# Kernel tuning notes

Hardware: AMD Instinct MI355X
Metric: run time of the kernel (lower is better)

Reference implementation:

```python
import jax, jax.numpy as jnp
import numpy as np

BS, SL, N_AGENTS, OBS_DIM, STATE_DIM, N_EDGES, HID = 32, 512, 32, 96, 1024, 64, 256


def _hgcn(w_line, x, H):
    # x: [B, n, 1]; H: [B, n, E]. Faithful to torch HGCN:
    # A = D^{-1/2} H |W| B^{-1} H^T D^{-1/2}, with D, B built from detached H/|W|,
    # inf entries (from 0^{-1} / 0^{-0.5}) zeroed. Diagonal matmuls are implicit scalings.
    w_abs = jnp.abs(w_line)
    Hd = jax.lax.stop_gradient(H)
    d = jnp.einsum('bne,e->bn', Hd, jax.lax.stop_gradient(w_abs))  # [B, n]
    d_is = jnp.where(d > 0, jax.lax.rsqrt(jnp.where(d > 0, d, 1.0)), 0.0)
    b = jnp.sum(Hd, axis=-2)  # [B, E]
    b_inv = jnp.where(b > 0, 1.0 / jnp.where(b > 0, b, 1.0), 0.0)
    t = d_is[..., None] * x                       # D^{-1/2} x
    s = jnp.einsum('bne,bnk->bek', H, t)          # H^T (...)
    s = s * (w_abs[None, :] * b_inv)[..., None]   # |W| B^{-1} (diagonals commute)
    y = jnp.einsum('bne,bek->bnk', H, s)          # H (...)
    return d_is[..., None] * y                    # D^{-1/2} (...)


def _mlp(x, w1, b1, w2, b2):
    return jax.nn.relu(x @ w1 + b1) @ w2 + b2


def setup_inputs() -> dict:
    key = jax.random.key(0)
    ks = jax.random.split(key, 24)
    f = jax.random.normal
    inp = {
        'agent_qs': f(ks[0], (BS, SL, N_AGENTS), jnp.float32),
        'states': f(ks[1], (BS, SL, STATE_DIM), jnp.float32),
        'indiv_us': f(ks[2], (BS, SL, N_AGENTS, OBS_DIM), jnp.float32),
        'edge_W': f(ks[3], (OBS_DIM, N_EDGES), jnp.float32) * 0.1,
        'edge_b': f(ks[4], (N_EDGES,), jnp.float32) * 0.1,
        'wline1': 1.0 + 0.1 * f(ks[5], (N_EDGES,), jnp.float32),
        'wline2': 1.0 + 0.1 * f(ks[6], (N_EDGES,), jnp.float32),
    }
    names = ['hw1', 'hc1', 'hw', 'hc']
    outs = [N_AGENTS, N_AGENTS, N_AGENTS, 1]
    for i, (nm, od) in enumerate(zip(names, outs)):
        inp[nm + '_w1'] = f(ks[7 + 4 * i], (STATE_DIM, HID), jnp.float32) * 0.05
        inp[nm + '_b1'] = f(ks[8 + 4 * i], (HID,), jnp.float32) * 0.05
        inp[nm + '_w2'] = f(ks[9 + 4 * i], (HID, od), jnp.float32) * 0.05
        inp[nm + '_b2'] = f(ks[10 + 4 * i], (od,), jnp.float32) * 0.05
    return inp


def reference(agent_qs, states, indiv_us, edge_W, edge_b, wline1, wline2,
              hw1_w1, hw1_b1, hw1_w2, hw1_b2, hc1_w1, hc1_b1, hc1_w2, hc1_b2,
              hw_w1, hw_b1, hw_w2, hw_b2, hc_w1, hc_b1, hc_w2, hc_b2):
    bs, sl, n = agent_qs.shape
    q = agent_qs.reshape(-1, n)                               # [B, n]
    u = indiv_us.reshape(-1, n, indiv_us.shape[-1])           # [B, n, obs]
    s = states.reshape(-1, states.shape[-1])                  # [B, state_dim]
    H = jax.nn.relu(u @ edge_W + edge_b)                      # hyper_edge_net -> [B, n, E]
    x = q[..., None]                                          # node_features [B, n, 1]
    qs_tot = _hgcn(wline2, _hgcn(wline1, x, H), H)[..., 0]    # two stacked HGCN encoders
    w1 = jnp.abs(_mlp(s, hw1_w1, hw1_b1, hw1_w2, hw1_b2))
    c1 = _mlp(s, hc1_w1, hc1_b1, hc1_w2, hc1_b2)
    qt = jax.nn.elu(qs_tot * w1 + c1)
    w = jnp.abs(_mlp(s, hw_w1, hw_b1, hw_w2, hw_b2))
    c = _mlp(s, hc_w1, hc_b1, hc_w2, hc_b2)[..., 0]
    q_tot = jnp.sum(qt * w, axis=-1) + c
    return q_tot.reshape(bs, sl, 1)
```

## Files before the change

### kernel.cpp

```cpp
#include <hip/hip_runtime.h>
#include <cstdint>

typedef _Float16 f16;
typedef _Float16 f16x2 __attribute__((ext_vector_type(2)));
typedef _Float16 f16x4 __attribute__((ext_vector_type(4)));
typedef _Float16 f16x8 __attribute__((ext_vector_type(8)));
typedef float f32x4 __attribute__((ext_vector_type(4)));

#define AS1U const __attribute__((address_space(1))) unsigned int
#define AS3U __attribute__((address_space(3))) unsigned int

__device__ __forceinline__ void gload_lds16(const void* g, void* l) {
    __builtin_amdgcn_global_load_lds((AS1U*)g, (AS3U*)l, 16, 0, 0);
}

#define WSYNC() asm volatile("s_waitcnt lgkmcnt(0)" ::: "memory")
#define CFENCE() asm volatile("" ::: "memory")

#define BATCH 16384
#define NAG   32
#define OBS   96
#define SDIM  1024
#define NE    64
#define HIDN  256
#define NH    1024

#define NB_ST 1024
#define NB_PW 256
#define NB_SM 101
#define NB_FRONT (NB_ST + NB_PW + NB_SM)

__global__ __launch_bounds__(256) void k_front(
    const float* __restrict__ states,
    const float* __restrict__ w1a, const float* __restrict__ w1b,
    const float* __restrict__ w1c, const float* __restrict__ w1d,
    const float* __restrict__ b1a, const float* __restrict__ b1b,
    const float* __restrict__ b1c, const float* __restrict__ b1d,
    const float* __restrict__ w2a, const float* __restrict__ w2b,
    const float* __restrict__ w2c, const float* __restrict__ w2d,
    f16* __restrict__ states16, f16* __restrict__ W1t, float* __restrict__ b1cat,
    f16* __restrict__ W2t, f16* __restrict__ hcw2) {
    __shared__ float tile[64 * 65];
    const int tid = threadIdx.x;
    int bid = blockIdx.x;

    if (bid < NB_ST) {
        int i = bid * 256 + tid;
        const int n4 = BATCH * SDIM / 4;
        const int stride = NB_ST * 256;
        for (; i < n4; i += stride) {
            float4 v = ((const float4*)states)[i];
            f16x4 h = { (f16)v.x, (f16)v.y, (f16)v.z, (f16)v.w };
            ((f16x4*)states16)[i] = h;
        }
        return;
    }
    bid -= NB_ST;
    if (bid < NB_PW) {
        int mlp = bid >> 6, rem = bid & 63, kt = rem >> 2, ct = rem & 3;
        const float* src = (mlp == 0) ? w1a : (mlp == 1) ? w1b : (mlp == 2) ? w1c : w1d;
        int k0 = kt * 64, c0 = ct * 64;
        for (int i = tid; i < 4096; i += 256) {
            int kk = i >> 6, cc = i & 63;
            tile[kk * 65 + cc] = src[(size_t)(k0 + kk) * 256 + c0 + cc];
        }
        __syncthreads();
        for (int i = tid; i < 4096; i += 256) {
            int cc = i >> 6, kk = i & 63;
            W1t[(size_t)(mlp * 256 + c0 + cc) * 1024 + k0 + kk] = (f16)tile[kk * 65 + cc];
        }
        return;
    }
    bid -= NB_PW;
    {
        int i = bid * 256 + tid;
        if (i < 24576) {
            int mp = i >> 13, rem = i & 8191, oo = rem >> 8, kk = rem & 255;
            const float* src = (mp == 0) ? w2a : (mp == 1) ? w2b : w2c;
            W2t[i] = (f16)src[kk * 32 + oo];
        } else if (i < 24832) {
            int k = i - 24576;
            hcw2[k] = (f16)w2d[k];
        } else if (i < 25856) {
            int n = i - 24832;
            int mlp = n >> 8, c = n & 255;
            const float* bsrc = (mlp == 0) ? b1a : (mlp == 1) ? b1b : (mlp == 2) ? b1c : b1d;
            b1cat[n] = bsrc[c];
        }
    }
}

__global__ __launch_bounds__(512) void k_gemm(
    const f16* __restrict__ A, const f16* __restrict__ B,
    const float* __restrict__ b1cat, const f16* __restrict__ W2t,
    const f16* __restrict__ hcw2, float* __restrict__ Pp) {
    __shared__ __align__(16) char smem[131072];
    f16* Asb = (f16*)smem;
    f16* Bsb = (f16*)(smem + 65536);
    f16* Ts  = (f16*)smem;

    const int tid = threadIdx.x;
    const int w = tid >> 6, l = tid & 63;
    const int lm = l & 15, lk = l >> 4;
    const int wm = w >> 2, wn = w & 3;
    const int p = blockIdx.x;
    const int xcd = p & 7, s = p >> 3;
    const int mt = xcd * 8 + (s >> 2);
    const int nt = s & 3;
    const int m0 = mt * 256, n0 = nt * 256;
    const int c0 = w * 4;
    const int srow = l >> 3;
    const int gchunk = (l & 7) ^ srow;

    float bj[4];
    #pragma unroll
    for (int j = 0; j < 4; j++) bj[j] = b1cat[n0 + wn * 64 + j * 16 + lm];

    f32x4 acc[8][4];
    #pragma unroll
    for (int i = 0; i < 8; i++)
        #pragma unroll
        for (int j = 0; j < 4; j++) acc[i][j] = (f32x4){0.f, 0.f, 0.f, 0.f};

#define STAGE(KT, BI)                                                                     \
    {                                                                                     \
        f16* Ad = Asb + (BI) * 16384;                                                     \
        f16* Bd = Bsb + (BI) * 16384;                                                     \
        _Pragma("unroll")                                                                 \
        for (int i_ = 0; i_ < 4; i_++) {                                                  \
            int cc = c0 + i_;                                                             \
            gload_lds16(&A[(size_t)(m0 + cc * 8 + srow) * 1024 + (KT) * 64 + gchunk * 8], \
                        &Ad[cc * 512]);                                                   \
            gload_lds16(&B[(size_t)(n0 + cc * 8 + srow) * 1024 + (KT) * 64 + gchunk * 8], \
                        &Bd[cc * 512]);                                                   \
        }                                                                                 \
    }

    STAGE(0, 0);
    STAGE(1, 1);

    for (int kt = 0; kt < 16; kt++) {
        if (kt < 15) { asm volatile("s_waitcnt vmcnt(8)" ::: "memory"); }
        else         { asm volatile("s_waitcnt vmcnt(0)" ::: "memory"); }
        CFENCE(); __builtin_amdgcn_s_barrier(); CFENCE();

        const f16* As_ = Asb + (kt & 1) * 16384;
        const f16* Bs_ = Bsb + (kt & 1) * 16384;
        const int swlo = ((lk ^ (lm & 7)) << 3);
        const int swhi = (((4 + lk) ^ (lm & 7)) << 3);

        f16x8 af[4][2], bf01[2][2], bf23[2][2];

        #pragma unroll
        for (int i = 0; i < 4; i++) {
            af[i][0] = *(const f16x8*)&As_[(wm * 128 + i * 16 + lm) * 64 + swlo];
            af[i][1] = *(const f16x8*)&As_[(wm * 128 + i * 16 + lm) * 64 + swhi];
        }
        #pragma unroll
        for (int j = 0; j < 2; j++) {
            bf01[j][0] = *(const f16x8*)&Bs_[(wn * 64 + j * 16 + lm) * 64 + swlo];
            bf01[j][1] = *(const f16x8*)&Bs_[(wn * 64 + j * 16 + lm) * 64 + swhi];
        }
        __builtin_amdgcn_s_setprio(1);
        #pragma unroll
        for (int ks = 0; ks < 2; ks++)
            #pragma unroll
            for (int i = 0; i < 4; i++)
                #pragma unroll
                for (int j = 0; j < 2; j++)
                    acc[i][j] = __builtin_amdgcn_mfma_f32_16x16x32_f16(af[i][ks], bf01[j][ks], acc[i][j], 0, 0, 0);
        __builtin_amdgcn_s_setprio(0);
        CFENCE(); __builtin_amdgcn_s_barrier(); CFENCE();

        #pragma unroll
        for (int j = 0; j < 2; j++) {
            bf23[j][0] = *(const f16x8*)&Bs_[(wn * 64 + (2 + j) * 16 + lm) * 64 + swlo];
            bf23[j][1] = *(const f16x8*)&Bs_[(wn * 64 + (2 + j) * 16 + lm) * 64 + swhi];
        }
        __builtin_amdgcn_s_setprio(1);
        #pragma unroll
        for (int ks = 0; ks < 2; ks++)
            #pragma unroll
            for (int i = 0; i < 4; i++)
                #pragma unroll
                for (int j = 0; j < 2; j++)
                    acc[i][2 + j] = __builtin_amdgcn_mfma_f32_16x16x32_f16(af[i][ks], bf23[j][ks], acc[i][2 + j], 0, 0, 0);
        __builtin_amdgcn_s_setprio(0);
        CFENCE(); __builtin_amdgcn_s_barrier(); CFENCE();

        #pragma unroll
        for (int i = 0; i < 4; i++) {
            af[i][0] = *(const f16x8*)&As_[(wm * 128 + (4 + i) * 16 + lm) * 64 + swlo];
            af[i][1] = *(const f16x8*)&As_[(wm * 128 + (4 + i) * 16 + lm) * 64 + swhi];
        }
        __builtin_amdgcn_s_setprio(1);
        #pragma unroll
        for (int ks = 0; ks < 2; ks++)
            #pragma unroll
            for (int i = 0; i < 4; i++)
                #pragma unroll
                for (int j = 0; j < 2; j++)
                    acc[4 + i][j] = __builtin_amdgcn_mfma_f32_16x16x32_f16(af[i][ks], bf01[j][ks], acc[4 + i][j], 0, 0, 0);
        __builtin_amdgcn_s_setprio(0);
        CFENCE(); __builtin_amdgcn_s_barrier(); CFENCE();

        if (kt < 14) STAGE(kt + 2, kt & 1);
        __builtin_amdgcn_s_setprio(1);
        #pragma unroll
        for (int ks = 0; ks < 2; ks++)
            #pragma unroll
            for (int i = 0; i < 4; i++)
                #pragma unroll
                for (int j = 0; j < 2; j++)
                    acc[4 + i][2 + j] = __builtin_amdgcn_mfma_f32_16x16x32_f16(af[i][ks], bf23[j][ks], acc[4 + i][2 + j], 0, 0, 0);
        __builtin_amdgcn_s_setprio(0);
    }
#undef STAGE

    __syncthreads();

    const int mlp = nt;
    #pragma unroll
    for (int pass = 0; pass < 2; pass++) {
        if (wm == pass) {
            #pragma unroll
            for (int i = 0; i < 8; i++)
                #pragma unroll
                for (int r = 0; r < 4; r++) {
                    int rl = i * 16 + lk * 4 + r;
                    #pragma unroll
                    for (int j = 0; j < 4; j++) {
                        float v = acc[i][j][r] + bj[j];
                        Ts[rl * 264 + wn * 64 + j * 16 + lm] = (f16)(v > 0.f ? v : 0.f);
                    }
                }
        }
        __syncthreads();
        const int grow = m0 + pass * 128 + w * 16;
        if (mlp < 3) {
            const f16* wb = W2t + mlp * 8192;
            f32x4 acc2[2];
            acc2[0] = (f32x4){0, 0, 0, 0}; acc2[1] = (f32x4){0, 0, 0, 0};
            #pragma unroll
            for (int ks = 0; ks < 8; ks++) {
                f16x8 a  = *(const f16x8*)&Ts[(w * 16 + lm) * 264 + ks * 32 + lk * 8];
                f16x8 b0 = *(const f16x8*)&wb[lm * 256 + ks * 32 + lk * 8];
                f16x8 b1 = *(const f16x8*)&wb[(16 + lm) * 256 + ks * 32 + lk * 8];
                acc2[0] = __builtin_amdgcn_mfma_f32_16x16x32_f16(a, b0, acc2[0], 0, 0, 0);
                acc2[1] = __builtin_amdgcn_mfma_f32_16x16x32_f16(a, b1, acc2[1], 0, 0, 0);
            }
            #pragma unroll
            for (int j2 = 0; j2 < 2; j2++)
                #pragma unroll
                for (int r = 0; r < 4; r++)
                    Pp[(size_t)(grow + lk * 4 + r) * 104 + mlp * 32 + j2 * 16 + lm] = acc2[j2][r];
        } else {
            f32x4 acc2 = (f32x4){0, 0, 0, 0};
            #pragma unroll
            for (int ks = 0; ks < 8; ks++) {
                f16x8 a = *(const f16x8*)&Ts[(w * 16 + lm) * 264 + ks * 32 + lk * 8];
                f16x8 bz = (f16x8){0, 0, 0, 0, 0, 0, 0, 0};
                if (lm == 0) bz = *(const f16x8*)&hcw2[ks * 32 + lk * 8];
                acc2 = __builtin_amdgcn_mfma_f32_16x16x32_f16(a, bz, acc2, 0, 0, 0);
            }
            if (lm == 0)
                #pragma unroll
                for (int r = 0; r < 4; r++)
                    Pp[(size_t)(grow + lk * 4 + r) * 104 + 96] = acc2[r];
        }
        if (pass == 0) __syncthreads();
    }
}

__global__ __launch_bounds__(256) void k_hgcn_ep(
    const float* __restrict__ agent_qs, const float* __restrict__ indiv_us,
    const float* __restrict__ edge_W, const float* __restrict__ edge_b,
    const float* __restrict__ wline1, const float* __restrict__ wline2,
    const float* __restrict__ Pp,
    const float* __restrict__ hw1_b2, const float* __restrict__ hc1_b2,
    const float* __restrict__ hw_b2, const float* __restrict__ hc_b2,
    float* __restrict__ out) {
    __shared__ __align__(16) char arena[34304];
    f16*   eWs   = (f16*)arena;
    float* swa   = (float*)(arena + 13312);
    f16*   HsB   = (f16*)(arena + 13824);
    float* svB   = (float*)(arena + 30720);
    float* sttB  = (float*)(arena + 31744);
    float* sdisB = (float*)(arena + 32256);
    float* sbinvB= (float*)(arena + 33280);

    const int tid = threadIdx.x;
    const int w = tid >> 6, l = tid & 63;
    const int b = blockIdx.x * 4 + w;
    f16*   Hw    = HsB + w * (32 * 66);
    float* sv    = svB + w * 64;
    float* stt   = sttB + w * 32;
    float* sdis  = sdisB + w * 64;
    float* sbinv = sbinvB + w * 64;

    const int nn = l & 31, half = l >> 5;

    float pa0 = 0.f, pc0 = 0.f, pw0 = 0.f;
    float p96a = 0.f, bw1 = 0.f, bc1 = 0.f, bww = 0.f, bhc = 0.f;
    if (half == 0) {
        const float* p0 = Pp + (size_t)b * 104;
        pa0 = p0[nn];
        pc0 = p0[32 + nn];
        pw0 = p0[64 + nn];
        p96a = p0[96];
        bw1 = hw1_b2[nn];  bc1 = hc1_b2[nn];
        bww = hw_b2[nn];   bhc = hc_b2[0];
    }
    float q = agent_qs[(size_t)b * 32 + nn];

    for (int i = tid; i < 6144; i += 256) {
        int k = i >> 6, n = i & 63;
        eWs[n * 104 + k] = (f16)edge_W[i];
    }
    if (tid < 64) swa[tid] = fabsf(wline1[tid]);
    else if (tid < 128) swa[tid] = fabsf(wline2[tid - 64]);
    __syncthreads();

    const int lm = l & 15, lk = l >> 4;
    const float* ub = indiv_us + (size_t)b * (NAG * OBS);

    #pragma unroll
    for (int mt = 0; mt < 2; mt++) {
        f16x8 af[3];
        #pragma unroll
        for (int ks = 0; ks < 3; ks++) {
            const float* up = ub + (mt * 16 + lm) * 96 + ks * 32 + lk * 8;
            float4 v0 = *(const float4*)up;
            float4 v1 = *(const float4*)(up + 4);
            af[ks] = (f16x8){ (f16)v0.x, (f16)v0.y, (f16)v0.z, (f16)v0.w,
                              (f16)v1.x, (f16)v1.y, (f16)v1.z, (f16)v1.w };
        }
        #pragma unroll
        for (int nt = 0; nt < 4; nt++) {
            f32x4 acc = {0.f, 0.f, 0.f, 0.f};
            #pragma unroll
            for (int ks = 0; ks < 3; ks++) {
                f16x8 bb = *(const f16x8*)&eWs[(nt * 16 + lm) * 104 + ks * 32 + lk * 8];
                acc = __builtin_amdgcn_mfma_f32_16x16x32_f16(af[ks], bb, acc, 0, 0, 0);
            }
            int col = nt * 16 + lm;
            float bias = edge_b[col];
            #pragma unroll
            for (int r = 0; r < 4; r++) {
                int row = mt * 16 + lk * 4 + r;
                float hv = acc[r] + bias;
                Hw[row * 66 + col] = (f16)(hv > 0.f ? hv : 0.f);
            }
        }
    }
    WSYNC();

    float bsum = 0.f;
    #pragma unroll
    for (int n = 0; n < 32; n++) bsum += (float)Hw[n * 66 + l];
    sbinv[l] = bsum > 0.f ? 1.f / bsum : 0.f;

    float dd = 0.f;
    #pragma unroll 8
    for (int e2 = 0; e2 < 32; e2++) {
        f16x2 h2 = *(const f16x2*)&Hw[nn * 66 + e2 * 2];
        dd += (float)h2.x * swa[half * 64 + e2 * 2] + (float)h2.y * swa[half * 64 + e2 * 2 + 1];
    }
    float dis = dd > 0.f ? rsqrtf(dd) : 0.f;
    sdis[l] = dis;
    if (half == 0) stt[nn] = dis * q;
    WSYNC();

    float s1 = 0.f;
    #pragma unroll
    for (int n = 0; n < 32; n++) s1 += (float)Hw[n * 66 + l] * stt[n];
    sv[l] = s1 * swa[l] * sbinv[l];
    WSYNC();

    float y1 = 0.f;
    #pragma unroll 8
    for (int e2 = 0; e2 < 32; e2++) {
        f16x2 h2 = *(const f16x2*)&Hw[nn * 66 + e2 * 2];
        y1 += (float)h2.x * sv[e2 * 2] + (float)h2.y * sv[e2 * 2 + 1];
    }
    float x2 = sdis[nn] * y1;
    if (half == 0) stt[nn] = sdis[32 + nn] * x2;
    WSYNC();

    float s2 = 0.f;
    #pragma unroll
    for (int n = 0; n < 32; n++) s2 += (float)Hw[n * 66 + l] * stt[n];
    sv[l] = s2 * swa[64 + l] * sbinv[l];
    WSYNC();

    float y2 = 0.f;
    #pragma unroll 8
    for (int e2 = 0; e2 < 32; e2++) {
        f16x2 h2 = *(const f16x2*)&Hw[nn * 66 + e2 * 2];
        y2 += (float)h2.x * sv[e2 * 2] + (float)h2.y * sv[e2 * 2 + 1];
    }

    float qsv = sdis[32 + nn] * y2;
    float w1v = fabsf(pa0 + bw1);
    float c1v = pc0 + bc1;
    float wwv = fabsf(pw0 + bww);
    float z = qsv * w1v + c1v;
    float qt = z > 0.f ? z : expm1f(z);
    float val = (half == 0) ? qt * wwv : 0.f;
    val += __shfl_xor(val, 1, 32);
    val += __shfl_xor(val, 2, 32);
    val += __shfl_xor(val, 4, 32);
    val += __shfl_xor(val, 8, 32);
    val += __shfl_xor(val, 16, 32);
    if (l == 0) out[b] = val + p96a + bhc;
}

extern "C" void kernel_launch(void* const* d_in, const int* in_sizes, int n_in,
                              void* d_out, int out_size, void* d_ws, size_t ws_size,
                              hipStream_t stream) {
    const float* agent_qs = (const float*)d_in[0];
    const float* states   = (const float*)d_in[1];
    const float* indiv_us = (const float*)d_in[2];
    const float* edge_W   = (const float*)d_in[3];
    const float* edge_b   = (const float*)d_in[4];
    const float* wline1   = (const float*)d_in[5];
    const float* wline2   = (const float*)d_in[6];
    const float* hw1_w1 = (const float*)d_in[7];
    const float* hw1_b1 = (const float*)d_in[8];
    const float* hw1_w2 = (const float*)d_in[9];
    const float* hw1_b2 = (const float*)d_in[10];
    const float* hc1_w1 = (const float*)d_in[11];
    const float* hc1_b1 = (const float*)d_in[12];
    const float* hc1_w2 = (const float*)d_in[13];
    const float* hc1_b2 = (const float*)d_in[14];
    const float* hw_w1  = (const float*)d_in[15];
    const float* hw_b1  = (const float*)d_in[16];
    const float* hw_w2  = (const float*)d_in[17];
    const float* hw_b2  = (const float*)d_in[18];
    const float* hc_w1  = (const float*)d_in[19];
    const float* hc_b1  = (const float*)d_in[20];
    const float* hc_w2  = (const float*)d_in[21];
    const float* hc_b2  = (const float*)d_in[22];

    char* ws = (char*)d_ws;
    size_t o_states16 = 0;
    size_t o_W1t  = o_states16 + (size_t)BATCH * SDIM * 2;
    size_t o_b1   = o_W1t + (size_t)NH * SDIM * 2;
    size_t o_W2t  = o_b1 + 4096;
    size_t o_hcw2 = o_W2t + 49152;
    size_t o_Pp   = o_hcw2 + 512;

    f16*   states16 = (f16*)(ws + o_states16);
    f16*   W1t      = (f16*)(ws + o_W1t);
    float* b1cat    = (float*)(ws + o_b1);
    f16*   W2t      = (f16*)(ws + o_W2t);
    f16*   hcw2     = (f16*)(ws + o_hcw2);
    float* Pp       = (float*)(ws + o_Pp);

    k_front<<<NB_FRONT, 256, 0, stream>>>(
        states,
        hw1_w1, hc1_w1, hw_w1, hc_w1, hw1_b1, hc1_b1, hw_b1, hc_b1,
        hw1_w2, hc1_w2, hw_w2, hc_w2,
        states16, W1t, b1cat, W2t, hcw2);
    k_gemm<<<256, 512, 0, stream>>>(states16, W1t, b1cat, W2t, hcw2, Pp);
    k_hgcn_ep<<<BATCH / 4, 256, 0, stream>>>(
        agent_qs, indiv_us, edge_W, edge_b, wline1, wline2, Pp,
        hw1_b2, hc1_b2, hw_b2, hc_b2, (float*)d_out);
}
```

Baseline: 120.4 us.

## Process four samples per wave in HGCN kernel with register prefetch

Each wave now handles four consecutive batch samples instead of one, with the grid shrunk accordingly. This amortizes the per-block edge_W conversion into LDS. While one sample is being computed, the indiv_us tile, Pp entries and agent_qs values for the next sample are loaded into registers so global latency overlaps compute. The cost is more live registers (48 floats for the prefetch buffer), which may lower occupancy, and fewer blocks to spread across the device.

New measurement: 131.5 us. 9.2% more time.

```diff
diff --git a/kernel.cpp b/kernel.cpp
--- a/kernel.cpp
+++ b/kernel.cpp
@@ -291,7 +291,7 @@
 
     const int tid = threadIdx.x;
     const int w = tid >> 6, l = tid & 63;
-    const int b = blockIdx.x * 4 + w;
+    const int b0 = blockIdx.x * 16 + w * 4;
     f16*   Hw    = HsB + w * (32 * 66);
     float* sv    = svB + w * 64;
     float* stt   = sttB + w * 32;
@@ -299,19 +299,28 @@
     float* sbinv = sbinvB + w * 64;
 
     const int nn = l & 31, half = l >> 5;
-
-    float pa0 = 0.f, pc0 = 0.f, pw0 = 0.f;
-    float p96a = 0.f, bw1 = 0.f, bc1 = 0.f, bww = 0.f, bhc = 0.f;
+    const int lm = l & 15, lk = l >> 4;
+
+    float4 uf[2][3][2];
+    {
+        const float* ub = indiv_us + (size_t)b0 * (NAG * OBS);
+        #pragma unroll
+        for (int mt = 0; mt < 2; mt++)
+            #pragma unroll
+            for (int ks = 0; ks < 3; ks++) {
+                const float* up = ub + (mt * 16 + lm) * 96 + ks * 32 + lk * 8;
+                uf[mt][ks][0] = *(const float4*)up;
+                uf[mt][ks][1] = *(const float4*)(up + 4);
+            }
+    }
+    float pa = 0.f, pc = 0.f, pw = 0.f, p96 = 0.f;
+    float bw1 = 0.f, bc1 = 0.f, bww = 0.f, bhc = 0.f;
     if (half == 0) {
-        const float* p0 = Pp + (size_t)b * 104;
-        pa0 = p0[nn];
-        pc0 = p0[32 + nn];
-        pw0 = p0[64 + nn];
-        p96a = p0[96];
-        bw1 = hw1_b2[nn];  bc1 = hc1_b2[nn];
-        bww = hw_b2[nn];   bhc = hc_b2[0];
-    }
-    float q = agent_qs[(size_t)b * 32 + nn];
+        const float* p0 = Pp + (size_t)b0 * 104;
+        pa = p0[nn]; pc = p0[32 + nn]; pw = p0[64 + nn]; p96 = p0[96];
+        bw1 = hw1_b2[nn]; bc1 = hc1_b2[nn]; bww = hw_b2[nn]; bhc = hc_b2[0];
+    }
+    float q = agent_qs[(size_t)b0 * 32 + nn];
 
     for (int i = tid; i < 6144; i += 256) {
         int k = i >> 6, n = i & 63;
@@ -321,98 +330,123 @@
     else if (tid < 128) swa[tid] = fabsf(wline2[tid - 64]);
     __syncthreads();
 
-    const int lm = l & 15, lk = l >> 4;
-    const float* ub = indiv_us + (size_t)b * (NAG * OBS);
-
     #pragma unroll
-    for (int mt = 0; mt < 2; mt++) {
-        f16x8 af[3];
-        #pragma unroll
-        for (int ks = 0; ks < 3; ks++) {
-            const float* up = ub + (mt * 16 + lm) * 96 + ks * 32 + lk * 8;
-            float4 v0 = *(const float4*)up;
-            float4 v1 = *(const float4*)(up + 4);
-            af[ks] = (f16x8){ (f16)v0.x, (f16)v0.y, (f16)v0.z, (f16)v0.w,
-                              (f16)v1.x, (f16)v1.y, (f16)v1.z, (f16)v1.w };
-        }
-        #pragma unroll
-        for (int nt = 0; nt < 4; nt++) {
-            f32x4 acc = {0.f, 0.f, 0.f, 0.f};
+    for (int it = 0; it < 4; it++) {
+        const int b = b0 + it;
+
+        f16x8 afc[2][3];
+        #pragma unroll
+        for (int mt = 0; mt < 2; mt++)
             #pragma unroll
             for (int ks = 0; ks < 3; ks++) {
-                f16x8 bb = *(const f16x8*)&eWs[(nt * 16 + lm) * 104 + ks * 32 + lk * 8];
-                acc = __builtin_amdgcn_mfma_f32_16x16x32_f16(af[ks], bb, acc, 0, 0, 0);
+                float4 v0 = uf[mt][ks][0], v1 = uf[mt][ks][1];
+                afc[mt][ks] = (f16x8){ (f16)v0.x, (f16)v0.y, (f16)v0.z, (f16)v0.w,
+                                       (f16)v1.x, (f16)v1.y, (f16)v1.z, (f16)v1.w };
             }
-            int col = nt * 16 + lm;
-            float bias = edge_b[col];
-            #pragma unroll
-            for (int r = 0; r < 4; r++) {
-                int row = mt * 16 + lk * 4 + r;
-                float hv = acc[r] + bias;
-                Hw[row * 66 + col] = (f16)(hv > 0.f ? hv : 0.f);
+
+        float pa_n = 0.f, pc_n = 0.f, pw_n = 0.f, p96_n = 0.f, q_n = 0.f;
+        if (it < 3) {
+            const float* ub = indiv_us + (size_t)(b + 1) * (NAG * OBS);
+            #pragma unroll
+            for (int mt = 0; mt < 2; mt++)
+                #pragma unroll
+                for (int ks = 0; ks < 3; ks++) {
+                    const float* up = ub + (mt * 16 + lm) * 96 + ks * 32 + lk * 8;
+                    uf[mt][ks][0] = *(const float4*)up;
+                    uf[mt][ks][1] = *(const float4*)(up + 4);
+                }
+            if (half == 0) {
+                const float* p0 = Pp + (size_t)(b + 1) * 104;
+                pa_n = p0[nn]; pc_n = p0[32 + nn]; pw_n = p0[64 + nn]; p96_n = p0[96];
             }
-        }
-    }
-    WSYNC();
-
-    float bsum = 0.f;
-    #pragma unroll
-    for (int n = 0; n < 32; n++) bsum += (float)Hw[n * 66 + l];
-    sbinv[l] = bsum > 0.f ? 1.f / bsum : 0.f;
-
-    float dd = 0.f;
-    #pragma unroll 8
-    for (int e2 = 0; e2 < 32; e2++) {
-        f16x2 h2 = *(const f16x2*)&Hw[nn * 66 + e2 * 2];
-        dd += (float)h2.x * swa[half * 64 + e2 * 2] + (float)h2.y * swa[half * 64 + e2 * 2 + 1];
-    }
-    float dis = dd > 0.f ? rsqrtf(dd) : 0.f;
-    sdis[l] = dis;
-    if (half == 0) stt[nn] = dis * q;
-    WSYNC();
-
-    float s1 = 0.f;
-    #pragma unroll
-    for (int n = 0; n < 32; n++) s1 += (float)Hw[n * 66 + l] * stt[n];
-    sv[l] = s1 * swa[l] * sbinv[l];
-    WSYNC();
-
-    float y1 = 0.f;
-    #pragma unroll 8
-    for (int e2 = 0; e2 < 32; e2++) {
-        f16x2 h2 = *(const f16x2*)&Hw[nn * 66 + e2 * 2];
-        y1 += (float)h2.x * sv[e2 * 2] + (float)h2.y * sv[e2 * 2 + 1];
-    }
-    float x2 = sdis[nn] * y1;
-    if (half == 0) stt[nn] = sdis[32 + nn] * x2;
-    WSYNC();
-
-    float s2 = 0.f;
-    #pragma unroll
-    for (int n = 0; n < 32; n++) s2 += (float)Hw[n * 66 + l] * stt[n];
-    sv[l] = s2 * swa[64 + l] * sbinv[l];
-    WSYNC();
-
-    float y2 = 0.f;
-    #pragma unroll 8
-    for (int e2 = 0; e2 < 32; e2++) {
-        f16x2 h2 = *(const f16x2*)&Hw[nn * 66 + e2 * 2];
-        y2 += (float)h2.x * sv[e2 * 2] + (float)h2.y * sv[e2 * 2 + 1];
-    }
-
-    float qsv = sdis[32 + nn] * y2;
-    float w1v = fabsf(pa0 + bw1);
-    float c1v = pc0 + bc1;
-    float wwv = fabsf(pw0 + bww);
-    float z = qsv * w1v + c1v;
-    float qt = z > 0.f ? z : expm1f(z);
-    float val = (half == 0) ? qt * wwv : 0.f;
-    val += __shfl_xor(val, 1, 32);
-    val += __shfl_xor(val, 2, 32);
-    val += __shfl_xor(val, 4, 32);
-    val += __shfl_xor(val, 8, 32);
-    val += __shfl_xor(val, 16, 32);
-    if (l == 0) out[b] = val + p96a + bhc;
+            q_n = agent_qs[(size_t)(b + 1) * 32 + nn];
+        }
+
+        #pragma unroll
+        for (int mt = 0; mt < 2; mt++) {
+            #pragma unroll
+            for (int nt = 0; nt < 4; nt++) {
+                f32x4 acc = {0.f, 0.f, 0.f, 0.f};
+                #pragma unroll
+                for (int ks = 0; ks < 3; ks++) {
+                    f16x8 bb = *(const f16x8*)&eWs[(nt * 16 + lm) * 104 + ks * 32 + lk * 8];
+                    acc = __builtin_amdgcn_mfma_f32_16x16x32_f16(afc[mt][ks], bb, acc, 0, 0, 0);
+                }
+                int col = nt * 16 + lm;
+                float bias = edge_b[col];
+                #pragma unroll
+                for (int r = 0; r < 4; r++) {
+                    int row = mt * 16 + lk * 4 + r;
+                    float hv = acc[r] + bias;
+                    Hw[row * 66 + col] = (f16)(hv > 0.f ? hv : 0.f);
+                }
+            }
+        }
+        WSYNC();
+
+        float bsum = 0.f;
+        #pragma unroll
+        for (int n = 0; n < 32; n++) bsum += (float)Hw[n * 66 + l];
+        sbinv[l] = bsum > 0.f ? 1.f / bsum : 0.f;
+
+        float dd = 0.f;
+        #pragma unroll 8
+        for (int e2 = 0; e2 < 32; e2++) {
+            f16x2 h2 = *(const f16x2*)&Hw[nn * 66 + e2 * 2];
+            dd += (float)h2.x * swa[half * 64 + e2 * 2] + (float)h2.y * swa[half * 64 + e2 * 2 + 1];
+        }
+        float dis = dd > 0.f ? rsqrtf(dd) : 0.f;
+        sdis[l] = dis;
+        if (half == 0) stt[nn] = dis * q;
+        WSYNC();
+
+        float s1 = 0.f;
+        #pragma unroll
+        for (int n = 0; n < 32; n++) s1 += (float)Hw[n * 66 + l] * stt[n];
+        sv[l] = s1 * swa[l] * sbinv[l];
+        WSYNC();
+
+        float y1 = 0.f;
+        #pragma unroll 8
+        for (int e2 = 0; e2 < 32; e2++) {
+            f16x2 h2 = *(const f16x2*)&Hw[nn * 66 + e2 * 2];
+            y1 += (float)h2.x * sv[e2 * 2] + (float)h2.y * sv[e2 * 2 + 1];
+        }
+        float x2 = sdis[nn] * y1;
+        if (half == 0) stt[nn] = sdis[32 + nn] * x2;
+        WSYNC();
+
+        float s2 = 0.f;
+        #pragma unroll
+        for (int n = 0; n < 32; n++) s2 += (float)Hw[n * 66 + l] * stt[n];
+        sv[l] = s2 * swa[64 + l] * sbinv[l];
+        WSYNC();
+
+        float y2 = 0.f;
+        #pragma unroll 8
+        for (int e2 = 0; e2 < 32; e2++) {
+            f16x2 h2 = *(const f16x2*)&Hw[nn * 66 + e2 * 2];
+            y2 += (float)h2.x * sv[e2 * 2] + (float)h2.y * sv[e2 * 2 + 1];
+        }
+
+        float qsv = sdis[32 + nn] * y2;
+        float w1v = fabsf(pa + bw1);
+        float c1v = pc + bc1;
+        float wwv = fabsf(pw + bww);
+        float z = qsv * w1v + c1v;
+        float qt = z > 0.f ? z : expm1f(z);
+        float val = (half == 0) ? qt * wwv : 0.f;
+        val += __shfl_xor(val, 1, 32);
+        val += __shfl_xor(val, 2, 32);
+        val += __shfl_xor(val, 4, 32);
+        val += __shfl_xor(val, 8, 32);
+        val += __shfl_xor(val, 16, 32);
+        if (l == 0) out[b] = val + p96 + bhc;
+
+        WSYNC();
+
+        pa = pa_n; pc = pc_n; pw = pw_n; p96 = p96_n; q = q_n;
+    }
 }
 
 extern "C" void kernel_launch(void* const* d_in, const int* in_sizes, int n_in,
@@ -463,7 +497,7 @@
         hw1_w2, hc1_w2, hw_w2, hc_w2,
         states16, W1t, b1cat, W2t, hcw2);
     k_gemm<<<256, 512, 0, stream>>>(states16, W1t, b1cat, W2t, hcw2, Pp);
-    k_hgcn_ep<<<BATCH / 4, 256, 0, stream>>>(
+    k_hgcn_ep<<<BATCH / 16, 256, 0, stream>>>(
         agent_qs, indiv_us, edge_W, edge_b, wline1, wline2, Pp,
         hw1_b2, hc1_b2, hw_b2, hc_b2, (float*)d_out);
 }
```

## Move HGCN into front kernel and shrink epilogue to a light combine

Applied to the files above, without the earlier changes.

The HGCN computation, which depends only on agent_qs, indiv_us and the hyperedge weights, now runs as extra blocks inside the first kernel alongside the state conversion and weight transposes, writing qs_tot to workspace. The final kernel becomes a small elementwise combine that reads Pp and qs_tot. The intent is to take the heavy HGCN work off the critical path after the GEMM and let it run concurrently with the front-stage work. The cost is an extra global round trip for qs_tot and a larger shared-memory arena for the front blocks, which may lower their occupancy.

Result: faster. 115.5 us (-4.1%).

```diff
diff --git a/kernel.cpp b/kernel.cpp
--- a/kernel.cpp
+++ b/kernel.cpp
@@ -25,13 +25,17 @@
 #define HIDN  256
 #define NH    1024
 
+#define NB_HG 4096
 #define NB_ST 1024
 #define NB_PW 256
 #define NB_SM 101
-#define NB_FRONT (NB_ST + NB_PW + NB_SM)
-
-__global__ __launch_bounds__(256) void k_front(
-    const float* __restrict__ states,
+#define NB_MAIN (NB_HG + NB_ST + NB_PW + NB_SM)
+
+__global__ __launch_bounds__(256) void k_main(
+    const float* __restrict__ agent_qs, const float* __restrict__ states,
+    const float* __restrict__ indiv_us, const float* __restrict__ edge_W,
+    const float* __restrict__ edge_b, const float* __restrict__ wline1,
+    const float* __restrict__ wline2,
     const float* __restrict__ w1a, const float* __restrict__ w1b,
     const float* __restrict__ w1c, const float* __restrict__ w1d,
     const float* __restrict__ b1a, const float* __restrict__ b1b,
@@ -39,10 +43,121 @@
     const float* __restrict__ w2a, const float* __restrict__ w2b,
     const float* __restrict__ w2c, const float* __restrict__ w2d,
     f16* __restrict__ states16, f16* __restrict__ W1t, float* __restrict__ b1cat,
-    f16* __restrict__ W2t, f16* __restrict__ hcw2) {
-    __shared__ float tile[64 * 65];
+    f16* __restrict__ W2t, f16* __restrict__ hcw2, float* __restrict__ qs_tot) {
+    __shared__ __align__(16) char arena[34304];
     const int tid = threadIdx.x;
     int bid = blockIdx.x;
+
+    if (bid < NB_HG) {
+        f16*   eWs   = (f16*)arena;
+        float* swa   = (float*)(arena + 13312);
+        f16*   HsB   = (f16*)(arena + 13824);
+        float* svB   = (float*)(arena + 30720);
+        float* sttB  = (float*)(arena + 31744);
+        float* sdisB = (float*)(arena + 32256);
+        float* sbinvB= (float*)(arena + 33280);
+
+        const int w = tid >> 6, l = tid & 63;
+        const int b = bid * 4 + w;
+        f16*   Hw    = HsB + w * (32 * 66);
+        float* sv    = svB + w * 64;
+        float* stt   = sttB + w * 32;
+        float* sdis  = sdisB + w * 64;
+        float* sbinv = sbinvB + w * 64;
+
+        const int nn = l & 31, half = l >> 5;
+        float q = agent_qs[(size_t)b * 32 + nn];
+
+        for (int i = tid; i < 6144; i += 256) {
+            int k = i >> 6, n = i & 63;
+            eWs[n * 104 + k] = (f16)edge_W[i];
+        }
+        if (tid < 64) swa[tid] = fabsf(wline1[tid]);
+        else if (tid < 128) swa[tid] = fabsf(wline2[tid - 64]);
+        __syncthreads();
+
+        const int lm = l & 15, lk = l >> 4;
+        const float* ub = indiv_us + (size_t)b * (NAG * OBS);
+
+        #pragma unroll
+        for (int mt = 0; mt < 2; mt++) {
+            f16x8 af[3];
+            #pragma unroll
+            for (int ks = 0; ks < 3; ks++) {
+                const float* up = ub + (mt * 16 + lm) * 96 + ks * 32 + lk * 8;
+                float4 v0 = *(const float4*)up;
+                float4 v1 = *(const float4*)(up + 4);
+                af[ks] = (f16x8){ (f16)v0.x, (f16)v0.y, (f16)v0.z, (f16)v0.w,
+                                  (f16)v1.x, (f16)v1.y, (f16)v1.z, (f16)v1.w };
+            }
+            #pragma unroll
+            for (int nt = 0; nt < 4; nt++) {
+                f32x4 acc = {0.f, 0.f, 0.f, 0.f};
+                #pragma unroll
+                for (int ks = 0; ks < 3; ks++) {
+                    f16x8 bb = *(const f16x8*)&eWs[(nt * 16 + lm) * 104 + ks * 32 + lk * 8];
+                    acc = __builtin_amdgcn_mfma_f32_16x16x32_f16(af[ks], bb, acc, 0, 0, 0);
+                }
+                int col = nt * 16 + lm;
+                float bias = edge_b[col];
+                #pragma unroll
+                for (int r = 0; r < 4; r++) {
+                    int row = mt * 16 + lk * 4 + r;
+                    float hv = acc[r] + bias;
+                    Hw[row * 66 + col] = (f16)(hv > 0.f ? hv : 0.f);
+                }
+            }
+        }
+        WSYNC();
+
+        float bsum = 0.f;
+        #pragma unroll
+        for (int n = 0; n < 32; n++) bsum += (float)Hw[n * 66 + l];
+        sbinv[l] = bsum > 0.f ? 1.f / bsum : 0.f;
+
+        float dd = 0.f;
+        #pragma unroll 8
+        for (int e2 = 0; e2 < 32; e2++) {
+            f16x2 h2 = *(const f16x2*)&Hw[nn * 66 + e2 * 2];
+            dd += (float)h2.x * swa[half * 64 + e2 * 2] + (float)h2.y * swa[half * 64 + e2 * 2 + 1];
+        }
+        float dis = dd > 0.f ? rsqrtf(dd) : 0.f;
+        sdis[l] = dis;
+        if (half == 0) stt[nn] = dis * q;
+        WSYNC();
+
+        float s1 = 0.f;
+        #pragma unroll
+        for (int n = 0; n < 32; n++) s1 += (float)Hw[n * 66 + l] * stt[n];
+        sv[l] = s1 * swa[l] * sbinv[l];
+        WSYNC();
+
+        float y1 = 0.f;
+        #pragma unroll 8
+        for (int e2 = 0; e2 < 32; e2++) {
+            f16x2 h2 = *(const f16x2*)&Hw[nn * 66 + e2 * 2];
+            y1 += (float)h2.x * sv[e2 * 2] + (float)h2.y * sv[e2 * 2 + 1];
+        }
+        float x2 = sdis[nn] * y1;
+        if (half == 0) stt[nn] = sdis[32 + nn] * x2;
+        WSYNC();
+
+        float s2 = 0.f;
+        #pragma unroll
+        for (int n = 0; n < 32; n++) s2 += (float)Hw[n * 66 + l] * stt[n];
+        sv[l] = s2 * swa[64 + l] * sbinv[l];
+        WSYNC();
+
+        float y2 = 0.f;
+        #pragma unroll 8
+        for (int e2 = 0; e2 < 32; e2++) {
+            f16x2 h2 = *(const f16x2*)&Hw[nn * 66 + e2 * 2];
+            y2 += (float)h2.x * sv[e2 * 2] + (float)h2.y * sv[e2 * 2 + 1];
+        }
+        if (half == 0) qs_tot[(size_t)b * 32 + nn] = sdis[32 + nn] * y2;
+        return;
+    }
+    bid -= NB_HG;
 
     if (bid < NB_ST) {
         int i = bid * 256 + tid;
@@ -57,6 +172,7 @@
     }
     bid -= NB_ST;
     if (bid < NB_PW) {
+        float* tile = (float*)arena;
         int mlp = bid >> 6, rem = bid & 63, kt = rem >> 2, ct = rem & 3;
         const float* src = (mlp == 0) ? w1a : (mlp == 1) ? w1b : (mlp == 2) ? w1c : w1d;
         int k0 = kt * 64, c0 = ct * 64;
@@ -272,147 +388,33 @@
     }
 }
 
-__global__ __launch_bounds__(256) void k_hgcn_ep(
-    const float* __restrict__ agent_qs, const float* __restrict__ indiv_us,
-    const float* __restrict__ edge_W, const float* __restrict__ edge_b,
-    const float* __restrict__ wline1, const float* __restrict__ wline2,
-    const float* __restrict__ Pp,
+__global__ __launch_bounds__(256) void k_ep(
+    const float* __restrict__ Pp, const float* __restrict__ qs_tot,
     const float* __restrict__ hw1_b2, const float* __restrict__ hc1_b2,
     const float* __restrict__ hw_b2, const float* __restrict__ hc_b2,
     float* __restrict__ out) {
-    __shared__ __align__(16) char arena[34304];
-    f16*   eWs   = (f16*)arena;
-    float* swa   = (float*)(arena + 13312);
-    f16*   HsB   = (f16*)(arena + 13824);
-    float* svB   = (float*)(arena + 30720);
-    float* sttB  = (float*)(arena + 31744);
-    float* sdisB = (float*)(arena + 32256);
-    float* sbinvB= (float*)(arena + 33280);
-
     const int tid = threadIdx.x;
-    const int w = tid >> 6, l = tid & 63;
-    const int b = blockIdx.x * 4 + w;
-    f16*   Hw    = HsB + w * (32 * 66);
-    float* sv    = svB + w * 64;
-    float* stt   = sttB + w * 32;
-    float* sdis  = sdisB + w * 64;
-    float* sbinv = sbinvB + w * 64;
-
-    const int nn = l & 31, half = l >> 5;
-
-    float pa0 = 0.f, pc0 = 0.f, pw0 = 0.f;
-    float p96a = 0.f, bw1 = 0.f, bc1 = 0.f, bww = 0.f, bhc = 0.f;
-    if (half == 0) {
-        const float* p0 = Pp + (size_t)b * 104;
-        pa0 = p0[nn];
-        pc0 = p0[32 + nn];
-        pw0 = p0[64 + nn];
-        p96a = p0[96];
-        bw1 = hw1_b2[nn];  bc1 = hc1_b2[nn];
-        bww = hw_b2[nn];   bhc = hc_b2[0];
-    }
-    float q = agent_qs[(size_t)b * 32 + nn];
-
-    for (int i = tid; i < 6144; i += 256) {
-        int k = i >> 6, n = i & 63;
-        eWs[n * 104 + k] = (f16)edge_W[i];
-    }
-    if (tid < 64) swa[tid] = fabsf(wline1[tid]);
-    else if (tid < 128) swa[tid] = fabsf(wline2[tid - 64]);
-    __syncthreads();
-
-    const int lm = l & 15, lk = l >> 4;
-    const float* ub = indiv_us + (size_t)b * (NAG * OBS);
-
+    const int row = blockIdx.x * 32 + (tid >> 3);
+    const int q8 = tid & 7, o = q8 * 4;
+    const float* p0 = Pp + (size_t)row * 104;
+    f32x4 a0 = *(const f32x4*)(p0 + o);
+    f32x4 c0 = *(const f32x4*)(p0 + 32 + o);
+    f32x4 w0 = *(const f32x4*)(p0 + 64 + o);
+    f32x4 qs = *(const f32x4*)(qs_tot + (size_t)row * 32 + o);
+    float val = 0.f;
     #pragma unroll
-    for (int mt = 0; mt < 2; mt++) {
-        f16x8 af[3];
-        #pragma unroll
-        for (int ks = 0; ks < 3; ks++) {
-            const float* up = ub + (mt * 16 + lm) * 96 + ks * 32 + lk * 8;
-            float4 v0 = *(const float4*)up;
-            float4 v1 = *(const float4*)(up + 4);
-            af[ks] = (f16x8){ (f16)v0.x, (f16)v0.y, (f16)v0.z, (f16)v0.w,
-                              (f16)v1.x, (f16)v1.y, (f16)v1.z, (f16)v1.w };
-        }
-        #pragma unroll
-        for (int nt = 0; nt < 4; nt++) {
-            f32x4 acc = {0.f, 0.f, 0.f, 0.f};
-            #pragma unroll
-            for (int ks = 0; ks < 3; ks++) {
-                f16x8 bb = *(const f16x8*)&eWs[(nt * 16 + lm) * 104 + ks * 32 + lk * 8];
-                acc = __builtin_amdgcn_mfma_f32_16x16x32_f16(af[ks], bb, acc, 0, 0, 0);
-            }
-            int col = nt * 16 + lm;
-            float bias = edge_b[col];
-            #pragma unroll
-            for (int r = 0; r < 4; r++) {
-                int row = mt * 16 + lk * 4 + r;
-                float hv = acc[r] + bias;
-                Hw[row * 66 + col] = (f16)(hv > 0.f ? hv : 0.f);
-            }
-        }
-    }
-    WSYNC();
-
-    float bsum = 0.f;
-    #pragma unroll
-    for (int n = 0; n < 32; n++) bsum += (float)Hw[n * 66 + l];
-    sbinv[l] = bsum > 0.f ? 1.f / bsum : 0.f;
-
-    float dd = 0.f;
-    #pragma unroll 8
-    for (int e2 = 0; e2 < 32; e2++) {
-        f16x2 h2 = *(const f16x2*)&Hw[nn * 66 + e2 * 2];
-        dd += (float)h2.x * swa[half * 64 + e2 * 2] + (float)h2.y * swa[half * 64 + e2 * 2 + 1];
-    }
-    float dis = dd > 0.f ? rsqrtf(dd) : 0.f;
-    sdis[l] = dis;
-    if (half == 0) stt[nn] = dis * q;
-    WSYNC();
-
-    float s1 = 0.f;
-    #pragma unroll
-    for (int n = 0; n < 32; n++) s1 += (float)Hw[n * 66 + l] * stt[n];
-    sv[l] = s1 * swa[l] * sbinv[l];
-    WSYNC();
-
-    float y1 = 0.f;
-    #pragma unroll 8
-    for (int e2 = 0; e2 < 32; e2++) {
-        f16x2 h2 = *(const f16x2*)&Hw[nn * 66 + e2 * 2];
-        y1 += (float)h2.x * sv[e2 * 2] + (float)h2.y * sv[e2 * 2 + 1];
-    }
-    float x2 = sdis[nn] * y1;
-    if (half == 0) stt[nn] = sdis[32 + nn] * x2;
-    WSYNC();
-
-    float s2 = 0.f;
-    #pragma unroll
-    for (int n = 0; n < 32; n++) s2 += (float)Hw[n * 66 + l] * stt[n];
-    sv[l] = s2 * swa[64 + l] * sbinv[l];
-    WSYNC();
-
-    float y2 = 0.f;
-    #pragma unroll 8
-    for (int e2 = 0; e2 < 32; e2++) {
-        f16x2 h2 = *(const f16x2*)&Hw[nn * 66 + e2 * 2];
-        y2 += (float)h2.x * sv[e2 * 2] + (float)h2.y * sv[e2 * 2 + 1];
-    }
-
-    float qsv = sdis[32 + nn] * y2;
-    float w1v = fabsf(pa0 + bw1);
-    float c1v = pc0 + bc1;
-    float wwv = fabsf(pw0 + bww);
-    float z = qsv * w1v + c1v;
-    float qt = z > 0.f ? z : expm1f(z);
-    float val = (half == 0) ? qt * wwv : 0.f;
-    val += __shfl_xor(val, 1, 32);
-    val += __shfl_xor(val, 2, 32);
-    val += __shfl_xor(val, 4, 32);
-    val += __shfl_xor(val, 8, 32);
-    val += __shfl_xor(val, 16, 32);
-    if (l == 0) out[b] = val + p96a + bhc;
+    for (int j = 0; j < 4; j++) {
+        float wv1 = fabsf(a0[j] + hw1_b2[o + j]);
+        float cv1 = c0[j] + hc1_b2[o + j];
+        float wv  = fabsf(w0[j] + hw_b2[o + j]);
+        float z = qs[j] * wv1 + cv1;
+        float qt = z > 0.f ? z : expm1f(z);
+        val += qt * wv;
+    }
+    val += __shfl_xor(val, 1);
+    val += __shfl_xor(val, 2);
+    val += __shfl_xor(val, 4);
+    if (q8 == 0) out[row] = val + p0[96] + hc_b2[0];
 }
 
 extern "C" void kernel_launch(void* const* d_in, const int* in_sizes, int n_in,
@@ -449,6 +451,7 @@
     size_t o_W2t  = o_b1 + 4096;
     size_t o_hcw2 = o_W2t + 49152;
     size_t o_Pp   = o_hcw2 + 512;
+    size_t o_qs   = o_Pp + (size_t)BATCH * 104 * 4;
 
     f16*   states16 = (f16*)(ws + o_states16);
     f16*   W1t      = (f16*)(ws + o_W1t);
@@ -456,14 +459,14 @@
     f16*   W2t      = (f16*)(ws + o_W2t);
     f16*   hcw2     = (f16*)(ws + o_hcw2);
     float* Pp       = (float*)(ws + o_Pp);
-
-    k_front<<<NB_FRONT, 256, 0, stream>>>(
-        states,
+    float* qs_tot   = (float*)(ws + o_qs);
+
+    k_main<<<NB_MAIN, 256, 0, stream>>>(
+        agent_qs, states, indiv_us, edge_W, edge_b, wline1, wline2,
         hw1_w1, hc1_w1, hw_w1, hc_w1, hw1_b1, hc1_b1, hw_b1, hc_b1,
         hw1_w2, hc1_w2, hw_w2, hc_w2,
-        states16, W1t, b1cat, W2t, hcw2);
+        states16, W1t, b1cat, W2t, hcw2, qs_tot);
     k_gemm<<<256, 512, 0, stream>>>(states16, W1t, b1cat, W2t, hcw2, Pp);
-    k_hgcn_ep<<<BATCH / 4, 256, 0, stream>>>(
-        agent_qs, indiv_us, edge_W, edge_b, wline1, wline2, Pp,
-        hw1_b2, hc1_b2, hw_b2, hc_b2, (float*)d_out);
+    k_ep<<<BATCH / 32, 256, 0, stream>>>(Pp, qs_tot, hw1_b2, hc1_b2, hw_b2, hc_b2,
+                                         (float*)d_out);
 }
```
